# Kernel optimization log

Hardware: AMD Instinct MI355X
Metric: run time of the kernel (lower is better)

The kernel has to match this reference:

```python
import jax, jax.numpy as jnp
import numpy as np

B, S, D, F, E, NS, K = 2, 2048, 512, 2048, 8, 2, 2


def setup_inputs() -> dict:
    key = jax.random.key(0)
    ks = jax.random.split(key, 6)
    scale = 0.02

    def p(k, shape):
        return jax.random.normal(k, shape, jnp.float32) * scale

    return {
        "x": jax.random.normal(ks[0], (B, S, D), jnp.float32),
        "gate_w": p(ks[1], (E, D)),
        "gate_b": jnp.zeros((E,), jnp.float32),
        "sw1": p(ks[2], (NS, F, D)),
        "sb1": jnp.zeros((NS, F), jnp.float32),
        "sw2": p(ks[3], (NS, D, F)),
        "sb2": jnp.zeros((NS, D), jnp.float32),
        "rw1": p(ks[4], (E, F, D)),
        "rb1": jnp.zeros((E, F), jnp.float32),
        "rw2": p(ks[5], (E, D, F)),
        "rb2": jnp.zeros((E, D), jnp.float32),
    }


def reference(x, gate_w, gate_b, sw1, sb1, sw2, sb2, rw1, rb1, rw2, rb2):
    b, s, d = x.shape
    t = x.reshape(-1, d)  # [T, D] flatten batch*seq tokens
    T = t.shape[0]

    # ---- shared experts: sum over NS FFNs (GELU exact, matching nn.GELU) ----
    hs = jax.nn.gelu(jnp.einsum('td,nfd->ntf', t, sw1) + sb1[:, None, :],
                     approximate=False)
    shared = jnp.einsum('ntf,ndf->td', hs, sw2) + sb2.sum(axis=0)

    # ---- router: softmax over experts, top-k probs/indices ----
    logits = t @ gate_w.T + gate_b               # [T, E]
    probs = jax.nn.softmax(logits, axis=-1)
    top_v, top_i = jax.lax.top_k(probs, K)       # [T, K]

    # combine weights: cw[t, e] = sum_k top_v[t, k] * (top_i[t, k] == e)
    cw = jnp.zeros_like(probs).at[jnp.arange(T)[:, None], top_i].add(top_v)  # [T, E]

    # ---- routed experts: run each expert FFN over all tokens, combine by cw ----
    # Mathematically identical to the masked gather/scatter loop in the source:
    # tokens with cw[t,e]==0 contribute nothing.
    hr = jax.nn.gelu(jnp.einsum('td,efd->etf', t, rw1) + rb1[:, None, :],
                     approximate=False)          # [E, T, F]
    oe = jnp.einsum('etf,edf->etd', hr, rw2) + rb2[:, None, :]  # [E, T, D]
    routed = jnp.einsum('etd,te->td', oe, cw)    # weighted combine

    return (shared + routed).reshape(b, s, d)
```

## Files before the change

### kernel.cpp

```cpp
#include <hip/hip_runtime.h>
#include <math.h>

typedef unsigned short u16;
typedef __attribute__((ext_vector_type(8))) __bf16 bf16x8;
typedef __attribute__((ext_vector_type(4))) float floatx4;

#define T_TOK 4096
#define DD    512
#define FF    2048
#define EE    8
#define NSH   2

#define BM 128
#define BN 128
#define BK 32
#define LDK 40
#define LDK2 32
#define BT2 64
#define CAP 4096
#define PADF 0x80000000u
#define NSLOT (2 * T_TOK + EE * BM)

__device__ __forceinline__ float bf2f(u16 v) {
  union { unsigned int u; float f; } c; c.u = ((unsigned int)v) << 16; return c.f;
}
__device__ __forceinline__ u16 f2bf(float f) {
  union { float ff; unsigned int u; } c; c.ff = f;
  unsigned int u = c.u;
  u += 0x7fffu + ((u >> 16) & 1u);
  return (u16)(u >> 16);
}
__device__ __forceinline__ float decode(const void* p, size_t idx, int f) {
  return f ? ((const float*)p)[idx] : bf2f(((const u16*)p)[idx]);
}
__device__ __forceinline__ bf16x8 load8(const void* base, size_t idx, int f) {
  if (f) {
    const float* p = (const float*)base + idx;
    float4 a = *(const float4*)p;
    float4 b = *(const float4*)(p + 4);
    union { bf16x8 v; u16 s[8]; } u;
    u.s[0] = f2bf(a.x); u.s[1] = f2bf(a.y); u.s[2] = f2bf(a.z); u.s[3] = f2bf(a.w);
    u.s[4] = f2bf(b.x); u.s[5] = f2bf(b.y); u.s[6] = f2bf(b.z); u.s[7] = f2bf(b.w);
    return u.v;
  }
  return *(const bf16x8*)((const u16*)base + idx);
}
__device__ __forceinline__ void loadf8(const void* p, size_t idx, int f,
                                       float* o) {
  if (f) {
    const float* q = (const float*)p + idx;
    float4 a = *(const float4*)q;
    float4 b = *(const float4*)(q + 4);
    o[0] = a.x; o[1] = a.y; o[2] = a.z; o[3] = a.w;
    o[4] = b.x; o[5] = b.y; o[6] = b.z; o[7] = b.w;
  } else {
    union { bf16x8 v; u16 s[8]; } u;
    u.v = *(const bf16x8*)((const u16*)p + idx);
#pragma unroll
    for (int j = 0; j < 8; ++j) o[j] = bf2f(u.s[j]);
  }
}

__device__ __forceinline__ float fast_gelu(float v) {
  float x  = v * 0.70710678118654752f;
  float ax = fabsf(x);
  float t  = __builtin_amdgcn_rcpf(fmaf(0.3275911f, ax, 1.0f));
  float p  = fmaf(t, 1.061405429f, -1.453152027f);
  p = fmaf(t, p, 1.421413741f);
  p = fmaf(t, p, -0.284496736f);
  p = fmaf(t, p, 0.254829592f);
  p = p * t;
  float e  = __expf(-ax * ax);
  float er = fmaf(-p, e, 1.0f);
  er = (x < 0.f) ? -er : er;
  return 0.5f * v * (1.0f + er);
}

__device__ __forceinline__ void gll16(const void* g, void* l) {
  __builtin_amdgcn_global_load_lds(
      (const __attribute__((address_space(1))) void*)g,
      (__attribute__((address_space(3))) void*)l, 16, 0, 0);
}
__device__ __forceinline__ void stage4(const u16* gA0, const u16* gA1,
                                       const u16* gB0, const u16* gB1,
                                       u16* Asb, u16* Bsb, int wave, int k0) {
  gll16(gA0 + k0, Asb + wave * 512);
  gll16(gA1 + k0, Asb + 2048 + wave * 512);
  gll16(gB0 + k0, Bsb + wave * 512);
  gll16(gB1 + k0, Bsb + 2048 + wave * 512);
}

__device__ __forceinline__ void core128(const u16* gA0, const u16* gA1,
                                        const u16* gB0, const u16* gB1,
                                        int K, u16* As, u16* Bs,
                                        floatx4 acc[4][4], int wave,
                                        int wm, int wn, int r, int q) {
  for (int k0 = 0; k0 < K; k0 += BK) {
    __syncthreads();
    stage4(gA0, gA1, gB0, gB1, As, Bs, wave, k0);
    __syncthreads();
    bf16x8 af[4], bfr[4];
#pragma unroll
    for (int mi = 0; mi < 4; ++mi)
      af[mi] = *(const bf16x8*)(As + (wm + mi * 16 + r) * LDK2 + q * 8);
#pragma unroll
    for (int ni = 0; ni < 4; ++ni)
      bfr[ni] = *(const bf16x8*)(Bs + (wn + ni * 16 + r) * LDK2 + q * 8);
#pragma unroll
    for (int mi = 0; mi < 4; ++mi)
#pragma unroll
      for (int ni = 0; ni < 4; ++ni)
        acc[mi][ni] = __builtin_amdgcn_mfma_f32_16x16x32_bf16(
            af[mi], bfr[ni], acc[mi][ni], 0, 0, 0);
  }
}

__global__ __launch_bounds__(256) void detect_kernel(
    const void* x, const void* gw, const void* sw1, const void* sw2,
    const void* rw1, const void* rw2, int* flags, int* meta) {
  __shared__ int cnt;
  __shared__ int sflags[6];
  const void* ptrs[6] = {x, gw, sw1, sw2, rw1, rw2};
  for (int tnum = 0; tnum < 6; ++tnum) {
    if (threadIdx.x == 0) cnt = 0;
    __syncthreads();
    const u16* p = (const u16*)ptrs[tnum];
    int local = 0;
    for (int i = threadIdx.x; i < 4096; i += 256) {
      unsigned ef = (p[i] >> 7) & 0xFFu;
      if (ef >= 0xE0u) ++local;
    }
    if (local) atomicAdd(&cnt, local);
    __syncthreads();
    if (threadIdx.x == 0) sflags[tnum] = (cnt >= 16) ? 1 : 0;
    __syncthreads();
  }
  if (threadIdx.x == 0) {
#pragma unroll
    for (int i = 0; i < 6; ++i) flags[i] = sflags[i];
    flags[6] = sflags[0];
    flags[7] = 0;
  }
  if (meta && threadIdx.x < 24) meta[threadIdx.x] = 0;
}

__global__ __launch_bounds__(256) void conv_kernel(
    const void* __restrict__ src, u16* __restrict__ dst,
    const int* __restrict__ flags, int idx, size_t n) {
  int f = flags[idx];
  if (!f) return;
  size_t i = ((size_t)blockIdx.x * 256 + threadIdx.x) * 8;
  if (i >= n) return;
  *(bf16x8*)(dst + i) = load8(src, i, f);
}

__global__ __launch_bounds__(256) void router_v(
    const void* __restrict__ x, const void* __restrict__ gw,
    const u16* __restrict__ gb, const int* __restrict__ flags,
    float* __restrict__ cw, int2* __restrict__ tix) {
  int wave = threadIdx.x >> 6, lane = threadIdx.x & 63;
  int t = blockIdx.x * 4 + wave;
  int fx = flags[0], fg = flags[1];
  float xf[8];
  loadf8(x, (size_t)t * DD + lane * 8, fx, xf);
  float acc[EE];
#pragma unroll
  for (int e = 0; e < EE; ++e) {
    float gf[8];
    loadf8(gw, (size_t)e * DD + lane * 8, fg, gf);
    float a = 0.f;
#pragma unroll
    for (int j = 0; j < 8; ++j) a = fmaf(xf[j], gf[j], a);
    acc[e] = a;
  }
#pragma unroll
  for (int e = 0; e < EE; ++e) {
    float v = acc[e];
#pragma unroll
    for (int off = 32; off > 0; off >>= 1) v += __shfl_xor(v, off, 64);
    acc[e] = v;
  }
  if (lane == 0) {
    float m = -1e30f;
#pragma unroll
    for (int e = 0; e < EE; ++e) {
      acc[e] += bf2f(gb[e]);
      m = fmaxf(m, acc[e]);
    }
    float p[EE], s = 0.f;
#pragma unroll
    for (int e = 0; e < EE; ++e) { p[e] = expf(acc[e] - m); s += p[e]; }
    int i1 = 0;
#pragma unroll
    for (int e = 1; e < EE; ++e) if (p[e] > p[i1]) i1 = e;
    int i2 = (i1 == 0) ? 1 : 0;
#pragma unroll
    for (int e = 0; e < EE; ++e)
      if (e != i1 && p[e] > p[i2]) i2 = e;
    float inv = 1.0f / s;
#pragma unroll
    for (int e = 0; e < EE; ++e)
      cw[t * EE + e] = (e == i1 || e == i2) ? p[e] * inv : 0.0f;
    tix[t] = make_int2(i1, i2);
  }
}

__global__ __launch_bounds__(256) void build_lists(
    const int2* __restrict__ tix, int* __restrict__ meta,
    unsigned* __restrict__ list, int4* __restrict__ srec) {
  int t = blockIdx.x * 256 + threadIdx.x;
  if (t >= T_TOK) return;
  int2 ii = tix[t];
  int p0 = atomicAdd(&meta[ii.x], 1);
  list[(size_t)ii.x * CAP + p0] = (unsigned)t;
  int p1 = atomicAdd(&meta[ii.y], 1);
  list[(size_t)ii.y * CAP + p1] = (unsigned)t;
  srec[t] = make_int4(ii.x, p0, ii.y, p1);
}
__global__ __launch_bounds__(256) void pad_lists(int* meta, unsigned* list) {
  if (threadIdx.x == 0) {
    int off = 0;
    for (int e = 0; e < EE; ++e) {
      int c = meta[e];
      int pc = (c + BM - 1) & ~(BM - 1);
      meta[8 + e] = pc;
      meta[16 + e] = off;
      off += pc;
    }
  }
  __syncthreads();
#pragma unroll
  for (int e = 0; e < EE; ++e) {
    int c = meta[e], pc = meta[8 + e];
    int i = c + threadIdx.x;
    if (i < pc) list[(size_t)e * CAP + i] = PADF;
  }
}


__global__ __launch_bounds__(256) void g1_fused(
    const void* __restrict__ xr, const u16* __restrict__ xb,
    const void* __restrict__ s1r, const u16* __restrict__ s1b,
    const u16* __restrict__ sb1,
    const void* __restrict__ r1r, const u16* __restrict__ r1b,
    const u16* __restrict__ rb1, const unsigned* __restrict__ list,
    const int* __restrict__ meta, const int* __restrict__ flags,
    u16* __restrict__ Hsh, u16* __restrict__ Hrt) {
  const u16* xp  = flags[0] ? xb  : (const u16*)xr;
  const u16* s1p = flags[2] ? s1b : (const u16*)s1r;
  const u16* r1p = flags[4] ? r1b : (const u16*)r1r;

  int z = blockIdx.z;
  int bm = blockIdx.y * BM;
  int tid = threadIdx.x, lane = tid & 63, wave = tid >> 6;
  int wm = (wave >> 1) * 64, wn = (wave & 1) * 64;
  int r = lane & 15, q = lane >> 4;
  int srow = tid >> 2, sc8 = (tid & 3) * 8;
  const int K = DD;

  __shared__ u16 As[BM * LDK2];
  __shared__ u16 Bs[BN * LDK2];

  const u16 *gA0, *gA1, *gB0;
  int e = 0, ho = 0, bn;
  if (z < 2) {
    bn = (z * 16 + blockIdx.x) * BN;
    gA0 = xp + (size_t)(bm + srow) * K + sc8;
    gA1 = gA0 + (size_t)64 * K;
    gB0 = s1p + (size_t)(bn + srow) * K + sc8;
  } else {
    e = z - 2;
    if (bm >= meta[8 + e]) return;
    ho = meta[16 + e];
    bn = blockIdx.x * BN;
    unsigned t0 = list[(size_t)e * CAP + bm + srow] & 0x7fffffffu;
    unsigned t1 = list[(size_t)e * CAP + bm + srow + 64] & 0x7fffffffu;
    gA0 = xp + (size_t)t0 * K + sc8;
    gA1 = xp + (size_t)t1 * K + sc8;
    gB0 = r1p + (size_t)e * FF * DD + (size_t)(bn + srow) * K + sc8;
  }
  const u16* gB1 = gB0 + (size_t)64 * K;

  floatx4 acc[4][4];
  floatx4 zero = {0.f, 0.f, 0.f, 0.f};
#pragma unroll
  for (int i = 0; i < 4; ++i)
#pragma unroll
    for (int j = 0; j < 4; ++j) acc[i][j] = zero;

  core128(gA0, gA1, gB0, gB1, K, As, Bs, acc, wave, wm, wn, r, q);

  if (z < 2) {
#pragma unroll
    for (int mi = 0; mi < 4; ++mi)
#pragma unroll
      for (int ni = 0; ni < 4; ++ni) {
        int col = bn + wn + ni * 16 + r;
        float bv = bf2f(sb1[col]);
#pragma unroll
        for (int rr = 0; rr < 4; ++rr) {
          int row = bm + wm + mi * 16 + q * 4 + rr;
          float v = acc[mi][ni][rr] + bv;
          Hsh[(size_t)row * (NSH * FF) + col] = f2bf(fast_gelu(v));
        }
      }
  } else {
#pragma unroll
    for (int mi = 0; mi < 4; ++mi)
#pragma unroll
      for (int ni = 0; ni < 4; ++ni) {
        int col = bn + wn + ni * 16 + r;
        float bv = bf2f(rb1[(size_t)e * FF + col]);
#pragma unroll
        for (int rr = 0; rr < 4; ++rr) {
          int slot = bm + wm + mi * 16 + q * 4 + rr;
          float v = acc[mi][ni][rr] + bv;
          Hrt[(size_t)(ho + slot) * FF + col] = f2bf(fast_gelu(v));
        }
      }
  }
}

__global__ __launch_bounds__(256) void g2_fused(
    const u16* __restrict__ Hsh,
    const void* __restrict__ s2r, const u16* __restrict__ s2b,
    const u16* __restrict__ sb2, const u16* __restrict__ Hrt,
    const void* __restrict__ r2r, const u16* __restrict__ r2b,
    const u16* __restrict__ rb2,
    const unsigned* __restrict__ list, const int* __restrict__ meta,
    const int* __restrict__ flags, const float* __restrict__ cw,
    float* __restrict__ oacc, float* __restrict__ Ort) {
  const u16* s2p = flags[3] ? s2b : (const u16*)s2r;
  const u16* r2p = flags[5] ? r2b : (const u16*)r2r;

  int z = blockIdx.z;
  int bm = blockIdx.y * BM;
  int bn = blockIdx.x * BN;
  int tid = threadIdx.x, lane = tid & 63, wave = tid >> 6;
  int wm = (wave >> 1) * 64, wn = (wave & 1) * 64;
  int r = lane & 15, q = lane >> 4;
  int srow = tid >> 2, sc8 = (tid & 3) * 8;
  const int K = FF;

  __shared__ u16 As[BM * LDK2];
  __shared__ u16 Bs[BN * LDK2];

  const u16 *gA0, *gA1, *gB0;
  int e = 0, ho = 0;
  if (z < NSH) {
    gA0 = Hsh + (size_t)(bm + srow) * (NSH * FF) + (size_t)z * FF + sc8;
    gA1 = gA0 + (size_t)64 * (NSH * FF);
    gB0 = s2p + (size_t)z * DD * FF + (size_t)(bn + srow) * K + sc8;
  } else {
    e = z - NSH;
    if (bm >= meta[8 + e]) return;
    ho = meta[16 + e];
    gA0 = Hrt + (size_t)(ho + bm + srow) * K + sc8;
    gA1 = gA0 + (size_t)64 * K;
    gB0 = r2p + (size_t)e * DD * FF + (size_t)(bn + srow) * K + sc8;
  }
  const u16* gB1 = gB0 + (size_t)64 * K;

  floatx4 acc[4][4];
  floatx4 zero = {0.f, 0.f, 0.f, 0.f};
#pragma unroll
  for (int i = 0; i < 4; ++i)
#pragma unroll
    for (int j = 0; j < 4; ++j) acc[i][j] = zero;

  core128(gA0, gA1, gB0, gB1, K, As, Bs, acc, wave, wm, wn, r, q);

  if (z < NSH) {
    float* op = oacc + (size_t)z * T_TOK * DD;
#pragma unroll
    for (int mi = 0; mi < 4; ++mi)
#pragma unroll
      for (int ni = 0; ni < 4; ++ni) {
        int col = bn + wn + ni * 16 + r;
        float bv = bf2f(sb2[(size_t)z * DD + col]);
#pragma unroll
        for (int rr = 0; rr < 4; ++rr) {
          int row = bm + wm + mi * 16 + q * 4 + rr;
          op[(size_t)row * DD + col] = acc[mi][ni][rr] + bv;
        }
      }
  } else {
#pragma unroll
    for (int mi = 0; mi < 4; ++mi)
#pragma unroll
      for (int rr = 0; rr < 4; ++rr) {
        int slot = bm + wm + mi * 16 + q * 4 + rr;
        unsigned raw = list[(size_t)e * CAP + slot];
        if (raw & PADF) continue;
        float s = cw[raw * EE + e];
#pragma unroll
        for (int ni = 0; ni < 4; ++ni) {
          int col = bn + wn + ni * 16 + r;
          float v = acc[mi][ni][rr] + bf2f(rb2[(size_t)e * DD + col]);
          Ort[(size_t)(ho + slot) * DD + col] = s * v;
        }
      }
  }
}

typedef struct { u16 a, b, c, d; } u16x4;
__global__ __launch_bounds__(256) void combine_out(
    const float* __restrict__ oacc, const float* __restrict__ Ort,
    const int4* __restrict__ srec, const int* __restrict__ meta,
    void* __restrict__ out, const int* __restrict__ flags) {
  int t  = blockIdx.x * 2 + (threadIdx.x >> 7);
  int c4 = (threadIdx.x & 127) * 4;
  int4 sr = srec[t];
  int g0 = meta[16 + sr.x] + sr.y;
  int g1 = meta[16 + sr.z] + sr.w;
  float4 a = *(const float4*)(oacc + (size_t)t * DD + c4);
  float4 b = *(const float4*)(oacc + (size_t)(T_TOK + t) * DD + c4);
  float4 u = *(const float4*)(Ort + (size_t)g0 * DD + c4);
  float4 v = *(const float4*)(Ort + (size_t)g1 * DD + c4);
  float o0 = a.x + b.x + u.x + v.x;
  float o1 = a.y + b.y + u.y + v.y;
  float o2 = a.z + b.z + u.z + v.z;
  float o3 = a.w + b.w + u.w + v.w;
  size_t idx = (size_t)t * DD + c4;
  if (flags[6]) {
    *(float4*)((float*)out + idx) = make_float4(o0, o1, o2, o3);
  } else {
    u16x4 h = {f2bf(o0), f2bf(o1), f2bf(o2), f2bf(o3)};
    *(u16x4*)((u16*)out + idx) = h;
  }
}

__device__ __forceinline__ void gemm_core(const void* A, size_t aoff, int fA,
                                          const void* B, size_t boff, int fB,
                                          int K, u16* As, u16* Bs,
                                          floatx4 acc[4][4]) {
  int tid  = threadIdx.x;
  int lane = tid & 63, wave = tid >> 6;
  int wm = (wave >> 1) * 64, wn = (wave & 1) * 64;
  int r = lane & 15, q = lane >> 4;
  int srow = tid >> 2;
  int sc8  = (tid & 3) * 8;
  size_t abase = aoff + (size_t)srow * K + sc8;
  size_t bbase = boff + (size_t)srow * K + sc8;
  const size_t half = (size_t)64 * K;

  for (int k0 = 0; k0 < K; k0 += BK) {
    bf16x8 av0 = load8(A, abase + k0, fA);
    bf16x8 av1 = load8(A, abase + half + k0, fA);
    bf16x8 bv0 = load8(B, bbase + k0, fB);
    bf16x8 bv1 = load8(B, bbase + half + k0, fB);
    __syncthreads();
    *(bf16x8*)(As + srow * LDK + sc8)        = av0;
    *(bf16x8*)(As + (srow + 64) * LDK + sc8) = av1;
    *(bf16x8*)(Bs + srow * LDK + sc8)        = bv0;
    *(bf16x8*)(Bs + (srow + 64) * LDK + sc8) = bv1;
    __syncthreads();

    bf16x8 af[4], bfr[4];
#pragma unroll
    for (int mi = 0; mi < 4; ++mi)
      af[mi] = *(const bf16x8*)(As + (wm + mi * 16 + r) * LDK + q * 8);
#pragma unroll
    for (int ni = 0; ni < 4; ++ni)
      bfr[ni] = *(const bf16x8*)(Bs + (wn + ni * 16 + r) * LDK + q * 8);
#pragma unroll
    for (int mi = 0; mi < 4; ++mi)
#pragma unroll
      for (int ni = 0; ni < 4; ++ni)
        acc[mi][ni] = __builtin_amdgcn_mfma_f32_16x16x32_bf16(
            af[mi], bfr[ni], acc[mi][ni], 0, 0, 0);
  }
}

__global__ __launch_bounds__(256) void gemm1_gelu(
    const void* __restrict__ A, size_t aoff, const void* __restrict__ B,
    size_t boff, const u16* __restrict__ bias, size_t bioff,
    u16* __restrict__ H, const int* __restrict__ flags, int iA, int iB,
    int N, int K) {
  __shared__ u16 As[BM * LDK];
  __shared__ u16 Bs[BN * LDK];
  int fA = flags[iA], fB = flags[iB];
  floatx4 acc[4][4];
  floatx4 zero = {0.f, 0.f, 0.f, 0.f};
#pragma unroll
  for (int i = 0; i < 4; ++i)
#pragma unroll
    for (int j = 0; j < 4; ++j) acc[i][j] = zero;

  int bm = blockIdx.y * BM, bn = blockIdx.x * BN;
  gemm_core(A, aoff + (size_t)bm * K, fA, B, boff + (size_t)bn * K, fB, K,
            As, Bs, acc);

  int tid = threadIdx.x, wave = tid >> 6, lane = tid & 63;
  int wm = (wave >> 1) * 64, wn = (wave & 1) * 64;
  int r = lane & 15, q = lane >> 4;
#pragma unroll
  for (int mi = 0; mi < 4; ++mi)
#pragma unroll
    for (int ni = 0; ni < 4; ++ni) {
      int col = bn + wn + ni * 16 + r;
      float bv = bf2f(bias[bioff + col]);
#pragma unroll
      for (int rr = 0; rr < 4; ++rr) {
        int row = bm + wm + mi * 16 + q * 4 + rr;
        float v = acc[mi][ni][rr] + bv;
        H[(size_t)row * N + col] = f2bf(fast_gelu(v));
      }
    }
}

__global__ __launch_bounds__(256) void gemm2_acc(
    const u16* __restrict__ A, const void* __restrict__ B, size_t boff,
    const u16* __restrict__ bias, size_t bioff, float* __restrict__ outf,
    void* __restrict__ outb, const float* __restrict__ cw,
    const int* __restrict__ flags, int iB, int expert, int accum,
    int row0, int N, int K) {
  __shared__ u16 As[BT2 * LDK];
  __shared__ u16 Bs[BT2 * LDK];
  int fB = flags[iB], fO = flags[6];
  floatx4 acc[2][2];
  floatx4 zero = {0.f, 0.f, 0.f, 0.f};
#pragma unroll
  for (int i = 0; i < 2; ++i)
#pragma unroll
    for (int j = 0; j < 2; ++j) acc[i][j] = zero;

  int bm = blockIdx.y * BT2, bn = blockIdx.x * BT2;
  int tid  = threadIdx.x;
  int lane = tid & 63, wave = tid >> 6;
  int wm = (wave >> 1) * 32, wn = (wave & 1) * 32;
  int r = lane & 15, q = lane >> 4;
  int srow = tid >> 2;
  int sc8  = (tid & 3) * 8;
  size_t abase = (size_t)(bm + srow) * K + sc8;
  size_t bbase = boff + (size_t)(bn + srow) * K + sc8;

  for (int k0 = 0; k0 < K; k0 += BK) {
    bf16x8 av = *(const bf16x8*)(A + abase + k0);
    bf16x8 bv = load8(B, bbase + k0, fB);
    __syncthreads();
    *(bf16x8*)(As + srow * LDK + sc8) = av;
    *(bf16x8*)(Bs + srow * LDK + sc8) = bv;
    __syncthreads();

    bf16x8 af[2], bfr[2];
#pragma unroll
    for (int mi = 0; mi < 2; ++mi)
      af[mi] = *(const bf16x8*)(As + (wm + mi * 16 + r) * LDK + q * 8);
#pragma unroll
    for (int ni = 0; ni < 2; ++ni)
      bfr[ni] = *(const bf16x8*)(Bs + (wn + ni * 16 + r) * LDK + q * 8);
#pragma unroll
    for (int mi = 0; mi < 2; ++mi)
#pragma unroll
      for (int ni = 0; ni < 2; ++ni)
        acc[mi][ni] = __builtin_amdgcn_mfma_f32_16x16x32_bf16(
            af[mi], bfr[ni], acc[mi][ni], 0, 0, 0);
  }

#pragma unroll
  for (int mi = 0; mi < 2; ++mi)
#pragma unroll
    for (int rr = 0; rr < 4; ++rr) {
      int grow = row0 + bm + wm + mi * 16 + q * 4 + rr;
      float s = cw ? cw[grow * EE + expert] : 1.0f;
#pragma unroll
      for (int ni = 0; ni < 2; ++ni) {
        int col = bn + wn + ni * 16 + r;
        float v = acc[mi][ni][rr] + bf2f(bias[bioff + col]);
        size_t idx = (size_t)grow * N + col;
        if (outf) {
          float prev = accum ? outf[idx] : 0.0f;
          outf[idx] = prev + s * v;
        } else if (fO) {
          float* ob = (float*)outb;
          float prev = accum ? ob[idx] : 0.0f;
          ob[idx] = prev + s * v;
        } else {
          u16* ob = (u16*)outb;
          float prev = accum ? bf2f(ob[idx]) : 0.0f;
          ob[idx] = f2bf(prev + s * v);
        }
      }
    }
}

__global__ __launch_bounds__(256) void convert_out(
    const float* __restrict__ acc, void* __restrict__ out,
    const int* __restrict__ flags, int n) {
  int i = blockIdx.x * blockDim.x + threadIdx.x;
  if (i >= n) return;
  if (flags[6]) ((float*)out)[i] = acc[i];
  else ((u16*)out)[i] = f2bf(acc[i]);
}

extern "C" void kernel_launch(void* const* d_in, const int* in_sizes, int n_in,
                              void* d_out, int out_size, void* d_ws, size_t ws_size,
                              hipStream_t stream) {
  (void)in_sizes; (void)n_in; (void)out_size;
  const void* x   = d_in[0];
  const void* gw  = d_in[1];
  const u16*  gb  = (const u16*)d_in[2];
  const void* sw1 = d_in[3];
  const u16*  sb1 = (const u16*)d_in[4];
  const void* sw2 = d_in[5];
  const u16*  sb2 = (const u16*)d_in[6];
  const void* rw1 = d_in[7];
  const u16*  rb1 = (const u16*)d_in[8];
  const void* rw2 = d_in[9];
  const u16*  rb2 = (const u16*)d_in[10];

  const size_t NX   = (size_t)T_TOK * DD;
  const size_t NW1S = (size_t)NSH * FF * DD;
  const size_t NW1R = (size_t)EE * FF * DD;
  const size_t NW2S = (size_t)NSH * DD * FF;
  const size_t NW2R = (size_t)EE * DD * FF;

  size_t off = 0;
  const size_t flO   = off; off += 256;
  const size_t cwO   = off; off += (size_t)T_TOK * EE * 4;
  const size_t tixO  = off; off += (size_t)T_TOK * 8;
  const size_t metaO = off; off += 256;
  const size_t listO = off; off += (size_t)EE * CAP * 4;
  const size_t srecO = off; off += (size_t)T_TOK * 16;
  const size_t accO  = off; off += (size_t)NSH * T_TOK * DD * 4;
  const size_t hshO  = off; off += (size_t)T_TOK * NSH * FF * 2;
  const size_t hrtO  = off; off += (size_t)NSLOT * FF * 2;
  const size_t ortO  = off; off += (size_t)NSLOT * DD * 4;
  const size_t xbO   = off; off += NX * 2;
  const size_t s1O   = off; off += NW1S * 2;
  const size_t r1O   = off; off += NW1R * 2;
  const size_t s2O   = off; off += NW2S * 2;
  const size_t r2O   = off; off += NW2R * 2;
  const int fast = (off <= ws_size) ? 1 : 0;

  char* ws = (char*)d_ws;
  int*   flags = (int*)(ws + flO);
  float* cw    = (float*)(ws + cwO);
  dim3 blk(256);

  if (fast) {
    int2*     tix  = (int2*)(ws + tixO);
    int*      meta = (int*)(ws + metaO);
    unsigned* list = (unsigned*)(ws + listO);
    int4*     srec = (int4*)(ws + srecO);
    float*    oacc = (float*)(ws + accO);
    u16*      Hsh  = (u16*)(ws + hshO);
    u16*      Hrt  = (u16*)(ws + hrtO);
    float*    Ort  = (float*)(ws + ortO);
    u16*      xb   = (u16*)(ws + xbO);
    u16*      s1b  = (u16*)(ws + s1O);
    u16*      r1b  = (u16*)(ws + r1O);
    u16*      s2b  = (u16*)(ws + s2O);
    u16*      r2b  = (u16*)(ws + r2O);

    detect_kernel<<<1, 256, 0, stream>>>(x, gw, sw1, sw2, rw1, rw2, flags,
                                         meta);
    conv_kernel<<<NX   / 2048, 256, 0, stream>>>(x,   xb,  flags, 0, NX);
    conv_kernel<<<NW1S / 2048, 256, 0, stream>>>(sw1, s1b, flags, 2, NW1S);
    conv_kernel<<<NW1R / 2048, 256, 0, stream>>>(rw1, r1b, flags, 4, NW1R);
    conv_kernel<<<NW2S / 2048, 256, 0, stream>>>(sw2, s2b, flags, 3, NW2S);
    conv_kernel<<<NW2R / 2048, 256, 0, stream>>>(rw2, r2b, flags, 5, NW2R);
    router_v<<<T_TOK / 4, 256, 0, stream>>>(x, gw, gb, flags, cw, tix);
    build_lists<<<T_TOK / 256, 256, 0, stream>>>(tix, meta, list, srec);
    pad_lists<<<1, 256, 0, stream>>>(meta, list);

    dim3 gf1(16, T_TOK / BM, 2 + EE);
    g1_fused<<<gf1, blk, 0, stream>>>(x, xb, sw1, s1b, sb1, rw1, r1b, rb1,
                                      list, meta, flags, Hsh, Hrt);
    dim3 gf2(DD / BN, CAP / BM, NSH + EE);
    g2_fused<<<gf2, blk, 0, stream>>>(Hsh, sw2, s2b, sb2, Hrt, rw2, r2b, rb2,
                                      list, meta, flags, cw, oacc, Ort);
    combine_out<<<T_TOK / 2, 256, 0, stream>>>(oacc, Ort, srec, meta, d_out,
                                               flags);
    return;
  }

  detect_kernel<<<1, 256, 0, stream>>>(x, gw, sw1, sw2, rw1, rw2, flags,
                                       nullptr);
  const size_t flB = 256, cwB = (size_t)T_TOK * EE * 4, tixB = (size_t)T_TOK * 8;
  const size_t accB = (size_t)T_TOK * DD * 4;
  static const int tcs[4] = {4096, 2048, 1024, 512};
  int TC = 0, use_f32 = 1;
  for (int i = 0; i < 4; ++i)
    if (flB + cwB + tixB + accB + (size_t)tcs[i] * FF * 2 <= ws_size) { TC = tcs[i]; break; }
  if (!TC) {
    use_f32 = 0;
    for (int i = 0; i < 4; ++i)
      if (flB + cwB + tixB + (size_t)tcs[i] * FF * 2 <= ws_size) { TC = tcs[i]; break; }
  }
  if (!TC) { TC = 512; use_f32 = 0; }

  int2*  tix     = (int2*)(ws + flB + cwB);
  float* out_acc = use_f32 ? (float*)(ws + flB + cwB + tixB) : nullptr;
  u16*   H       = (u16*)(ws + flB + cwB + tixB + (use_f32 ? accB : 0));

  router_v<<<T_TOK / 4, 256, 0, stream>>>(x, gw, gb, flags, cw, tix);
  dim3 g1(FF / BN, TC / BM);
  dim3 g2(DD / BT2, TC / BT2);
  const int nchunk = T_TOK / TC;
  for (int f = 0; f < NSH + EE; ++f) {
    const void *w1, *w2; const u16 *b1, *b2; const float* cwp;
    int expert, i1, i2v; size_t w1off, w2off, b1off, b2off;
    if (f < NSH) {
      w1 = sw1; w2 = sw2; b1 = sb1; b2 = sb2;
      w1off = (size_t)f * FF * DD; w2off = (size_t)f * DD * FF;
      b1off = (size_t)f * FF; b2off = (size_t)f * DD;
      cwp = nullptr; expert = 0; i1 = 2; i2v = 3;
    } else {
      int e = f - NSH;
      w1 = rw1; w2 = rw2; b1 = rb1; b2 = rb2;
      w1off = (size_t)e * FF * DD; w2off = (size_t)e * DD * FF;
      b1off = (size_t)e * FF; b2off = (size_t)e * DD;
      cwp = cw; expert = e; i1 = 4; i2v = 5;
    }
    int accum = (f > 0) ? 1 : 0;
    for (int c = 0; c < nchunk; ++c) {
      size_t t0 = (size_t)c * TC;
      gemm1_gelu<<<g1, blk, 0, stream>>>(x, t0 * DD, w1, w1off, b1, b1off, H,
                                         flags, 0, i1, FF, DD);
      gemm2_acc<<<g2, blk, 0, stream>>>(H, w2, w2off, b2, b2off, out_acc,
                                        d_out, cwp, flags, i2v, expert, accum,
                                        (int)t0, DD, FF);
    }
  }
  if (use_f32)
    convert_out<<<(T_TOK * DD) / 256, 256, 0, stream>>>(out_acc, d_out, flags,
                                                        T_TOK * DD);
}
```

Measured before the change: 369.8 us.

## Double GEMM K-tile to 64 with XOR-swizzled LDS layout

The shared GEMM core now stages a 64-wide K slice per iteration instead of 32, which halves the number of barrier pairs per tile. It also stores rows in LDS with an XOR swizzle on the 16-byte chunk index, applied on the global-to-LDS load side and matched on the fragment reads. The swizzle is meant to remove LDS bank conflicts that the unpadded 32-element row stride caused. In exchange LDS usage per block doubles to 32 KB, which may reduce occupancy, and there is still no double buffering to overlap loads with MFMA work.

```diff
diff --git a/kernel.cpp b/kernel.cpp
--- a/kernel.cpp
+++ b/kernel.cpp
@@ -15,7 +15,6 @@
 #define BN 128
 #define BK 32
 #define LDK 40
-#define LDK2 32
 #define BT2 64
 #define CAP 4096
 #define PADF 0x80000000u
@@ -81,37 +80,47 @@
       (const __attribute__((address_space(1))) void*)g,
       (__attribute__((address_space(3))) void*)l, 16, 0, 0);
 }
-__device__ __forceinline__ void stage4(const u16* gA0, const u16* gA1,
-                                       const u16* gB0, const u16* gB1,
-                                       u16* Asb, u16* Bsb, int wave, int k0) {
-  gll16(gA0 + k0, Asb + wave * 512);
-  gll16(gA1 + k0, Asb + 2048 + wave * 512);
-  gll16(gB0 + k0, Bsb + wave * 512);
-  gll16(gB1 + k0, Bsb + 2048 + wave * 512);
-}
-
-__device__ __forceinline__ void core128(const u16* gA0, const u16* gA1,
-                                        const u16* gB0, const u16* gB1,
-                                        int K, u16* As, u16* Bs,
-                                        floatx4 acc[4][4], int wave,
-                                        int wm, int wn, int r, int q) {
-  for (int k0 = 0; k0 < K; k0 += BK) {
-    __syncthreads();
-    stage4(gA0, gA1, gB0, gB1, As, Bs, wave, k0);
-    __syncthreads();
-    bf16x8 af[4], bfr[4];
-#pragma unroll
-    for (int mi = 0; mi < 4; ++mi)
-      af[mi] = *(const bf16x8*)(As + (wm + mi * 16 + r) * LDK2 + q * 8);
-#pragma unroll
-    for (int ni = 0; ni < 4; ++ni)
-      bfr[ni] = *(const bf16x8*)(Bs + (wn + ni * 16 + r) * LDK2 + q * 8);
-#pragma unroll
-    for (int mi = 0; mi < 4; ++mi)
-#pragma unroll
-      for (int ni = 0; ni < 4; ++ni)
-        acc[mi][ni] = __builtin_amdgcn_mfma_f32_16x16x32_bf16(
-            af[mi], bfr[ni], acc[mi][ni], 0, 0, 0);
+
+#define BK2 64
+__device__ __forceinline__ void core128swz(
+    const u16* gA0, const u16* gA1, const u16* gA2, const u16* gA3,
+    const u16* gB0, const u16* gB1, const u16* gB2, const u16* gB3,
+    int K, u16* As, u16* Bs, floatx4 acc[4][4],
+    int wave, int wm, int wn, int r, int q) {
+  const int rs = r & 7;
+  for (int k0 = 0; k0 < K; k0 += BK2) {
+    __syncthreads();
+    gll16(gA0 + k0, As + wave * 512);
+    gll16(gA1 + k0, As + 2048 + wave * 512);
+    gll16(gA2 + k0, As + 4096 + wave * 512);
+    gll16(gA3 + k0, As + 6144 + wave * 512);
+    gll16(gB0 + k0, Bs + wave * 512);
+    gll16(gB1 + k0, Bs + 2048 + wave * 512);
+    gll16(gB2 + k0, Bs + 4096 + wave * 512);
+    gll16(gB3 + k0, Bs + 6144 + wave * 512);
+    __syncthreads();
+#pragma unroll
+    for (int s = 0; s < 2; ++s) {
+      bf16x8 af[4], bfr[4];
+#pragma unroll
+      for (int mi = 0; mi < 4; ++mi) {
+        int R = wm + mi * 16 + r;
+        int u = (s * 4 + q) ^ rs;
+        af[mi] = *(const bf16x8*)(As + R * 64 + u * 8);
+      }
+#pragma unroll
+      for (int ni = 0; ni < 4; ++ni) {
+        int R = wn + ni * 16 + r;
+        int u = (s * 4 + q) ^ rs;
+        bfr[ni] = *(const bf16x8*)(Bs + R * 64 + u * 8);
+      }
+#pragma unroll
+      for (int mi = 0; mi < 4; ++mi)
+#pragma unroll
+        for (int ni = 0; ni < 4; ++ni)
+          acc[mi][ni] = __builtin_amdgcn_mfma_f32_16x16x32_bf16(
+              af[mi], bfr[ni], acc[mi][ni], 0, 0, 0);
+    }
   }
 }
 
@@ -255,31 +264,36 @@
   int tid = threadIdx.x, lane = tid & 63, wave = tid >> 6;
   int wm = (wave >> 1) * 64, wn = (wave & 1) * 64;
   int r = lane & 15, q = lane >> 4;
-  int srow = tid >> 2, sc8 = (tid & 3) * 8;
   const int K = DD;
 
-  __shared__ u16 As[BM * LDK2];
-  __shared__ u16 Bs[BN * LDK2];
-
-  const u16 *gA0, *gA1, *gB0;
+  int rsub = tid >> 3;
+  int us = (tid & 7) ^ (rsub & 7);
+
+  __shared__ u16 As[BM * BK2];
+  __shared__ u16 Bs[BN * BK2];
+
+  const u16 *gA[4], *gB[4];
   int e = 0, ho = 0, bn;
   if (z < 2) {
     bn = (z * 16 + blockIdx.x) * BN;
-    gA0 = xp + (size_t)(bm + srow) * K + sc8;
-    gA1 = gA0 + (size_t)64 * K;
-    gB0 = s1p + (size_t)(bn + srow) * K + sc8;
+#pragma unroll
+    for (int c = 0; c < 4; ++c) {
+      gA[c] = xp + (size_t)(bm + c * 32 + rsub) * K + us * 8;
+      gB[c] = s1p + (size_t)(bn + c * 32 + rsub) * K + us * 8;
+    }
   } else {
     e = z - 2;
     if (bm >= meta[8 + e]) return;
     ho = meta[16 + e];
     bn = blockIdx.x * BN;
-    unsigned t0 = list[(size_t)e * CAP + bm + srow] & 0x7fffffffu;
-    unsigned t1 = list[(size_t)e * CAP + bm + srow + 64] & 0x7fffffffu;
-    gA0 = xp + (size_t)t0 * K + sc8;
-    gA1 = xp + (size_t)t1 * K + sc8;
-    gB0 = r1p + (size_t)e * FF * DD + (size_t)(bn + srow) * K + sc8;
-  }
-  const u16* gB1 = gB0 + (size_t)64 * K;
+#pragma unroll
+    for (int c = 0; c < 4; ++c) {
+      unsigned tk = list[(size_t)e * CAP + bm + c * 32 + rsub] & 0x7fffffffu;
+      gA[c] = xp + (size_t)tk * K + us * 8;
+      gB[c] = r1p + (size_t)e * FF * DD + (size_t)(bn + c * 32 + rsub) * K +
+              us * 8;
+    }
+  }
 
   floatx4 acc[4][4];
   floatx4 zero = {0.f, 0.f, 0.f, 0.f};
@@ -288,7 +302,8 @@
 #pragma unroll
     for (int j = 0; j < 4; ++j) acc[i][j] = zero;
 
-  core128(gA0, gA1, gB0, gB1, K, As, Bs, acc, wave, wm, wn, r, q);
+  core128swz(gA[0], gA[1], gA[2], gA[3], gB[0], gB[1], gB[2], gB[3],
+             K, As, Bs, acc, wave, wm, wn, r, q);
 
   if (z < 2) {
 #pragma unroll
@@ -339,27 +354,36 @@
   int tid = threadIdx.x, lane = tid & 63, wave = tid >> 6;
   int wm = (wave >> 1) * 64, wn = (wave & 1) * 64;
   int r = lane & 15, q = lane >> 4;
-  int srow = tid >> 2, sc8 = (tid & 3) * 8;
   const int K = FF;
 
-  __shared__ u16 As[BM * LDK2];
-  __shared__ u16 Bs[BN * LDK2];
-
-  const u16 *gA0, *gA1, *gB0;
+  int rsub = tid >> 3;
+  int us = (tid & 7) ^ (rsub & 7);
+
+  __shared__ u16 As[BM * BK2];
+  __shared__ u16 Bs[BN * BK2];
+
+  const u16 *gA[4], *gB[4];
   int e = 0, ho = 0;
   if (z < NSH) {
-    gA0 = Hsh + (size_t)(bm + srow) * (NSH * FF) + (size_t)z * FF + sc8;
-    gA1 = gA0 + (size_t)64 * (NSH * FF);
-    gB0 = s2p + (size_t)z * DD * FF + (size_t)(bn + srow) * K + sc8;
+    const int ldA = NSH * FF;
+#pragma unroll
+    for (int c = 0; c < 4; ++c) {
+      gA[c] = Hsh + (size_t)(bm + c * 32 + rsub) * ldA + (size_t)z * FF +
+              us * 8;
+      gB[c] = s2p + (size_t)z * DD * FF + (size_t)(bn + c * 32 + rsub) * K +
+              us * 8;
+    }
   } else {
     e = z - NSH;
     if (bm >= meta[8 + e]) return;
     ho = meta[16 + e];
-    gA0 = Hrt + (size_t)(ho + bm + srow) * K + sc8;
-    gA1 = gA0 + (size_t)64 * K;
-    gB0 = r2p + (size_t)e * DD * FF + (size_t)(bn + srow) * K + sc8;
-  }
-  const u16* gB1 = gB0 + (size_t)64 * K;
+#pragma unroll
+    for (int c = 0; c < 4; ++c) {
+      gA[c] = Hrt + (size_t)(ho + bm + c * 32 + rsub) * K + us * 8;
+      gB[c] = r2p + (size_t)e * DD * FF + (size_t)(bn + c * 32 + rsub) * K +
+              us * 8;
+    }
+  }
 
   floatx4 acc[4][4];
   floatx4 zero = {0.f, 0.f, 0.f, 0.f};
@@ -368,7 +392,8 @@
 #pragma unroll
     for (int j = 0; j < 4; ++j) acc[i][j] = zero;
 
-  core128(gA0, gA1, gB0, gB1, K, As, Bs, acc, wave, wm, wn, r, q);
+  core128swz(gA[0], gA[1], gA[2], gA[3], gB[0], gB[1], gB[2], gB[3],
+             K, As, Bs, acc, wave, wm, wn, r, q);
 
   if (z < NSH) {
     float* op = oacc + (size_t)z * T_TOK * DD;
```

Measured after the change: 375.5 us. Within noise of the previous version (+1.5%).
